# Optimization experiments

Hardware: AMD Instinct MI355X
Metric: run time of the kernel (lower is better)

## Reference

```python
import jax, jax.numpy as jnp
import numpy as np

N_NODES = 100000
IN_CH = 512
OUT_CH = 64
N_EDGES = 1600000
NEG_SLOPE = 0.2  # PyG GATv2Conv default negative_slope


def setup_inputs() -> dict:
    key = jax.random.key(0)
    ks = jax.random.split(key, 8)
    x = jax.random.normal(ks[0], (N_NODES, IN_CH), dtype=jnp.float32)
    edge_index = jax.random.randint(ks[1], (2, N_EDGES), 0, N_NODES, dtype=jnp.int64)
    s_in = 1.0 / np.sqrt(IN_CH)
    s_out = 1.0 / np.sqrt(OUT_CH)
    W_l = jax.random.uniform(ks[2], (IN_CH, OUT_CH), jnp.float32, -s_in, s_in)
    b_l = jnp.zeros((OUT_CH,), jnp.float32)
    W_r = jax.random.uniform(ks[3], (IN_CH, OUT_CH), jnp.float32, -s_in, s_in)
    b_r = jnp.zeros((OUT_CH,), jnp.float32)
    att = jax.random.uniform(ks[4], (OUT_CH,), jnp.float32, -s_out, s_out)
    bias = jnp.zeros((OUT_CH,), jnp.float32)
    return {"x": x, "edge_index": edge_index, "W_l": W_l, "b_l": b_l,
            "W_r": W_r, "b_r": b_r, "att": att, "bias": bias}


def reference(x, edge_index, W_l, b_l, W_r, b_r, att, bias):
    n = x.shape[0]
    # add self loops (PyG GATv2Conv default add_self_loops=True)
    loop = jnp.arange(n, dtype=edge_index.dtype)
    src = jnp.concatenate([edge_index[0], loop])  # source j
    dst = jnp.concatenate([edge_index[1], loop])  # target i

    x_l = x @ W_l + b_l  # [N, D] source-side transform
    x_r = x @ W_r + b_r  # [N, D] target-side transform

    # GATv2 attention logit per edge: att . LeakyReLU(x_l[j] + x_r[i])
    z = x_l[src] + x_r[dst]                       # [E, D]
    z = jnp.where(z > 0, z, NEG_SLOPE * z)
    logits = z @ att                               # [E]

    # segment softmax over incoming edges of each target node
    seg_max = jax.ops.segment_max(logits, dst, num_segments=n)
    seg_max = jnp.where(jnp.isfinite(seg_max), seg_max, 0.0)
    e = jnp.exp(logits - seg_max[dst])
    denom = jax.ops.segment_sum(e, dst, num_segments=n)
    alpha = e / jnp.maximum(denom[dst], 1e-16)     # [E]

    # weighted scatter-add aggregation of source features
    out = jax.ops.segment_sum(alpha[:, None] * x_l[src], dst, num_segments=n)
    return out + bias
```

## Files before the change

### kernel.cpp

```cpp
#include <hip/hip_runtime.h>
#include <hip/hip_bf16.h>

constexpr int IC = 512;
constexpr int OC = 64;
#define NEG_SLOPE 0.2f

constexpr int EPB = 4096;
constexpr int NBK = 128;
constexpr int BKSHIFT = 10;
constexpr int BKSIZE = 1024;

typedef __attribute__((ext_vector_type(8))) __bf16 bf16x8;
typedef __attribute__((ext_vector_type(4))) float f32x4;
typedef unsigned short u16;

__device__ __forceinline__ float bf2f(u16 h) {
  return __uint_as_float(((unsigned)h) << 16);
}

__global__ __launch_bounds__(256)
void k_shuffleB(const float* __restrict__ Wl, const float* __restrict__ Wr,
                __hip_bfloat16* __restrict__ Bp) {
  const int tid = blockIdx.x * 256 + threadIdx.x;
  if (tid >= 8 * 16 * 64) return;
  const int lane = tid & 63;
  const int kb = (tid >> 6) & 15;
  const int cb = tid >> 10;
  const int col = cb * 16 + (lane & 15);
  const int k0 = kb * 32 + (lane >> 4) * 8;
  const float* W = (col < OC) ? (Wl + col) : (Wr + (col - OC));
  bf16x8 v;
  #pragma unroll
  for (int j = 0; j < 8; ++j) v[j] = (__bf16)W[(size_t)(k0 + j) * OC];
  *(bf16x8*)(Bp + (size_t)tid * 8) = v;
}

__device__ inline bf16x8 cvt8(const float4& a, const float4& b) {
  bf16x8 r;
  r[0] = (__bf16)a.x; r[1] = (__bf16)a.y; r[2] = (__bf16)a.z; r[3] = (__bf16)a.w;
  r[4] = (__bf16)b.x; r[5] = (__bf16)b.y; r[6] = (__bf16)b.z; r[7] = (__bf16)b.w;
  return r;
}

__device__ __forceinline__ void gload_lds16(const float* g, const float* l) {
  __builtin_amdgcn_global_load_lds(
      (const __attribute__((address_space(1))) float*)(uintptr_t)g,
      (__attribute__((address_space(3))) float*)(uintptr_t)l,
      16, 0, 0);
}

__global__ __launch_bounds__(256)
void k_gemm(const float* __restrict__ x, const __hip_bfloat16* __restrict__ Bp,
            const float* __restrict__ bl, const float* __restrict__ br,
            __bf16* __restrict__ xl, __bf16* __restrict__ xr, int n) {
  __shared__ float As[2][128 * 64];
  const int t = threadIdx.x;
  const int lane = t & 63;
  const int w = t >> 6;
  const int l15 = lane & 15, lg = lane >> 4;
  const int rowbase_g = blockIdx.x * 128 + w * 32;

  const float* srcp[8];
  #pragma unroll
  for (int j = 0; j < 8; ++j) {
    const int row_l = w * 32 + j * 4 + lg;
    const int grow = min(blockIdx.x * 128 + row_l, n - 1);
    const int gch = l15 ^ ((j * 4 + lg) & 15);
    srcp[j] = x + (size_t)grow * IC + gch * 4;
  }
  const bf16x8* pb = (const bf16x8*)Bp + lane;

  f32x4 acc[2][8] = {};

  #pragma unroll
  for (int j = 0; j < 8; ++j)
    gload_lds16(srcp[j], &As[0][w * 2048 + j * 256]);

  int buf = 0;
  for (int kt = 0; kt < 8; ++kt) {
    bf16x8 bfr[2][8];
    #pragma unroll
    for (int kb = 0; kb < 2; ++kb)
      #pragma unroll
      for (int cb = 0; cb < 8; ++cb)
        bfr[kb][cb] = pb[(cb * 16 + kt * 2 + kb) * 64];
    asm volatile("s_waitcnt vmcnt(16)" ::: "memory");
    if (kt < 7) {
      #pragma unroll
      for (int j = 0; j < 8; ++j)
        gload_lds16(srcp[j] + (kt + 1) * 64, &As[buf ^ 1][w * 2048 + j * 256]);
    }
    #pragma unroll
    for (int kb = 0; kb < 2; ++kb) {
      const int kc0 = kb * 8 + lg * 2;
      const int s0 = (kc0 ^ l15) * 4;
      const int s1 = ((kc0 + 1) ^ l15) * 4;
      #pragma unroll
      for (int rg = 0; rg < 2; ++rg) {
        const int rbase = (w * 32 + rg * 16 + l15) * 64;
        const float4 f0 = *(const float4*)&As[buf][rbase + s0];
        const float4 f1 = *(const float4*)&As[buf][rbase + s1];
        const bf16x8 af = cvt8(f0, f1);
        #pragma unroll
        for (int cb = 0; cb < 8; ++cb)
          acc[rg][cb] = __builtin_amdgcn_mfma_f32_16x16x32_bf16(af, bfr[kb][cb], acc[rg][cb], 0, 0, 0);
      }
    }
    buf ^= 1;
  }

  #pragma unroll
  for (int cb = 0; cb < 8; ++cb) {
    const int col = cb * 16 + l15;
    __bf16* dst = (col < OC) ? xl : xr;
    const int c2 = col & (OC - 1);
    const float bv = (col < OC) ? bl[c2] : br[c2];
    #pragma unroll
    for (int rg = 0; rg < 2; ++rg) {
      const int rb = rowbase_g + rg * 16 + lg * 4;
      #pragma unroll
      for (int q = 0; q < 4; ++q)
        if (rb + q < n) dst[(size_t)(rb + q) * OC + c2] = (__bf16)(acc[rg][cb][q] + bv);
    }
  }
}

__global__ __launch_bounds__(256)
void k_bin1a(const int* __restrict__ edst, int* __restrict__ slen,
             int E, int nch) {
  __shared__ int lcnt[NBK];
  const int t = threadIdx.x;
  const int c = blockIdx.x;
  const int e0 = c * EPB;
  if (t < NBK) lcnt[t] = 0;
  __syncthreads();
  #pragma unroll
  for (int j = 0; j < 16; ++j) {
    const int i = e0 + j * 256 + t;
    if (i < E) atomicAdd(&lcnt[edst[i] >> BKSHIFT], 1);
  }
  __syncthreads();
  if (t < NBK) slen[t * nch + c] = lcnt[t];
}

__global__ __launch_bounds__(256)
void k_colscan(int* __restrict__ slen, int* __restrict__ btot, int nch) {
  __shared__ int sm[256];
  const int t = threadIdx.x;
  const int base = blockIdx.x * nch;
  const int per = (nch + 255) / 256;
  int v[8];
  int s = 0;
  for (int k = 0; k < per; ++k) {
    const int idx = t * per + k;
    v[k] = (idx < nch) ? slen[base + idx] : 0;
    s += v[k];
  }
  sm[t] = s;
  __syncthreads();
  #pragma unroll
  for (int d = 1; d < 256; d <<= 1) {
    int u = (t >= d) ? sm[t - d] : 0;
    __syncthreads();
    sm[t] += u;
    __syncthreads();
  }
  int run = (t == 0) ? 0 : sm[t - 1];
  for (int k = 0; k < per; ++k) {
    const int idx = t * per + k;
    if (idx < nch) slen[base + idx] = run;
    run += v[k];
  }
  if (t == 255) btot[blockIdx.x] = sm[255];
}

__global__ __launch_bounds__(256)
void k_bscan(const int* __restrict__ btot, int* __restrict__ bbase, int nbk) {
  __shared__ int sm[256];
  const int t = threadIdx.x;
  const int v = (t < nbk) ? btot[t] : 0;
  sm[t] = v;
  __syncthreads();
  #pragma unroll
  for (int d = 1; d < 256; d <<= 1) {
    int u = (t >= d) ? sm[t - d] : 0;
    __syncthreads();
    sm[t] += u;
    __syncthreads();
  }
  if (t < NBK) bbase[t] = sm[t] - v;
  if (t == NBK - 1) bbase[NBK] = sm[t];
}

__global__ __launch_bounds__(256)
void k_bin1b(const int* __restrict__ esrc, const int* __restrict__ edst,
             const int* __restrict__ slen, const int* __restrict__ bbase,
             int* __restrict__ bstage, int E, int nch) {
  __shared__ int lcnt[NBK];
  __shared__ int lbase[NBK];
  __shared__ int ldst[NBK];
  __shared__ int lword[EPB];
  __shared__ unsigned char lbkt[EPB];
  __shared__ int sm[256];
  const int t = threadIdx.x;
  const int c = blockIdx.x;
  const int e0 = c * EPB;
  if (t < NBK) lcnt[t] = 0;
  __syncthreads();

  int s_[16], d_[16], r_[16];
  #pragma unroll
  for (int j = 0; j < 16; ++j) {
    const int i = e0 + j * 256 + t;
    if (i < E) {
      s_[j] = esrc[i];
      d_[j] = edst[i];
      r_[j] = atomicAdd(&lcnt[d_[j] >> BKSHIFT], 1);
    }
  }
  __syncthreads();
  const int vv = (t < NBK) ? lcnt[t] : 0;
  sm[t] = vv;
  __syncthreads();
  #pragma unroll
  for (int d = 1; d < 256; d <<= 1) {
    int u = (t >= d) ? sm[t - d] : 0;
    __syncthreads();
    sm[t] += u;
    __syncthreads();
  }
  if (t < NBK) {
    lbase[t] = sm[t] - vv;
    ldst[t] = bbase[t] + slen[t * nch + c];
  }
  __syncthreads();
  #pragma unroll
  for (int j = 0; j < 16; ++j) {
    const int i = e0 + j * 256 + t;
    if (i < E) {
      const int b = d_[j] >> BKSHIFT;
      const int pos = lbase[b] + r_[j];
      lword[pos] = (s_[j] << BKSHIFT) | (d_[j] & (BKSIZE - 1));
      lbkt[pos] = (unsigned char)b;
    }
  }
  __syncthreads();
  const int used = min(E - e0, EPB);
  for (int k = t; k < used; k += 256) {
    const int b = lbkt[k];
    bstage[ldst[b] + (k - lbase[b])] = lword[k];
  }
}

__global__ __launch_bounds__(1024)
void k_boff(const int* __restrict__ bstage, const int* __restrict__ bbase,
            int* __restrict__ off, int n, int nbk) {
  __shared__ int lc[BKSIZE];
  __shared__ int sw[16];
  const int t = threadIdx.x;
  const int b = blockIdx.x;
  const int node0 = b << BKSHIFT;
  lc[t] = 0;
  __syncthreads();
  const int end = bbase[b + 1];
  for (int k = bbase[b] + t; k < end; k += 1024)
    atomicAdd(&lc[bstage[k] & (BKSIZE - 1)], 1);
  __syncthreads();
  const int v = lc[t];
  int sc = v;
  #pragma unroll
  for (int d = 1; d < 64; d <<= 1) {
    const int u = __shfl_up(sc, d);
    if ((t & 63) >= d) sc += u;
  }
  if ((t & 63) == 63) sw[t >> 6] = sc;
  __syncthreads();
  if (t < 64) {
    int s2 = (t < 16) ? sw[t] : 0;
    #pragma unroll
    for (int d = 1; d < 16; d <<= 1) {
      const int u = __shfl_up(s2, d);
      if (t >= d) s2 += u;
    }
    if (t < 16) sw[t] = s2;
  }
  __syncthreads();
  const int wbase = (t >= 64) ? sw[(t >> 6) - 1] : 0;
  const int node = node0 + t;
  if (node < n) off[node] = bbase[b] + node0 + t + (wbase + sc - v);
  if (b == nbk - 1 && t == 1023) off[n] = bbase[nbk] + n;
}

__global__ __launch_bounds__(1024)
void k_bplace(const int* __restrict__ bstage, const int* __restrict__ bbase,
              const int* __restrict__ off, int* __restrict__ rec, int n) {
  __shared__ int lcur[BKSIZE];
  const int t = threadIdx.x;
  const int b = blockIdx.x;
  const int node0 = b << BKSHIFT;
  if (node0 + t < n) {
    const int o = off[node0 + t];
    rec[o] = node0 + t;
    lcur[t] = o + 1;
  }
  __syncthreads();
  const int end = bbase[b + 1];
  for (int k = bbase[b] + t; k < end; k += 1024) {
    const int w = bstage[k];
    const int pos = atomicAdd(&lcur[w & (BKSIZE - 1)], 1);
    rec[pos] = w >> BKSHIFT;
  }
}

__global__ __launch_bounds__(256)
void k_gather(const int* __restrict__ off, const int* __restrict__ rec,
              const u16* __restrict__ xl, const u16* __restrict__ xr,
              const float* __restrict__ att, const float* __restrict__ bias,
              float* __restrict__ out, int n) {
  const int lane = threadIdx.x & 63;
  const int node = (blockIdx.x * 256 + threadIdx.x) >> 6;
  if (node >= n) return;
  const int slot = lane >> 4;
  const int c4 = (lane & 15) * 4;

  const ushort4 xrh = *(const ushort4*)(xr + (size_t)node * OC + c4);
  const float4 xrv = make_float4(bf2f(xrh.x), bf2f(xrh.y), bf2f(xrh.z), bf2f(xrh.w));
  const float4 aw  = *(const float4*)(att + c4);

  const int beg = off[node];
  const int end = off[node + 1];
  float denom = 0.0f;
  float4 acc = make_float4(0.f, 0.f, 0.f, 0.f);

  int p = beg + slot;
  bool cv = (p < end);
  ushort4 xh = make_ushort4(0, 0, 0, 0);
  if (cv) {
    const int s = rec[p];
    xh = *(const ushort4*)(xl + (size_t)s * OC + c4);
  }
  for (int base = beg; base < end; base += 4) {
    const ushort4 ch = xh;
    const bool curv = cv;
    p += 4;
    cv = (p < end);
    if (cv) {
      const int s = rec[p];
      xh = *(const ushort4*)(xl + (size_t)s * OC + c4);
    } else {
      xh = make_ushort4(0, 0, 0, 0);
    }
    const float4 cur = make_float4(bf2f(ch.x), bf2f(ch.y), bf2f(ch.z), bf2f(ch.w));
    float zx = cur.x + xrv.x; zx = zx > 0.f ? zx : NEG_SLOPE * zx;
    float zy = cur.y + xrv.y; zy = zy > 0.f ? zy : NEG_SLOPE * zy;
    float zz = cur.z + xrv.z; zz = zz > 0.f ? zz : NEG_SLOPE * zz;
    float zw = cur.w + xrv.w; zw = zw > 0.f ? zw : NEG_SLOPE * zw;
    float lg = zx * aw.x + zy * aw.y + zz * aw.z + zw * aw.w;
    lg += __shfl_xor(lg, 1);
    lg += __shfl_xor(lg, 2);
    lg += __shfl_xor(lg, 4);
    lg += __shfl_xor(lg, 8);
    const float wgt = curv ? __expf(lg) : 0.0f;
    denom += wgt;
    acc.x = fmaf(wgt, cur.x, acc.x);
    acc.y = fmaf(wgt, cur.y, acc.y);
    acc.z = fmaf(wgt, cur.z, acc.z);
    acc.w = fmaf(wgt, cur.w, acc.w);
  }
  denom += __shfl_xor(denom, 16);
  denom += __shfl_xor(denom, 32);
  acc.x += __shfl_xor(acc.x, 16); acc.x += __shfl_xor(acc.x, 32);
  acc.y += __shfl_xor(acc.y, 16); acc.y += __shfl_xor(acc.y, 32);
  acc.z += __shfl_xor(acc.z, 16); acc.z += __shfl_xor(acc.z, 32);
  acc.w += __shfl_xor(acc.w, 16); acc.w += __shfl_xor(acc.w, 32);

  if (slot == 0) {
    const float4 bv = *(const float4*)(bias + c4);
    const float inv = 1.0f / denom;
    float4 o;
    o.x = acc.x * inv + bv.x;
    o.y = acc.y * inv + bv.y;
    o.z = acc.z * inv + bv.z;
    o.w = acc.w * inv + bv.w;
    *(float4*)(out + (size_t)node * OC + c4) = o;
  }
}

extern "C" void kernel_launch(void* const* d_in, const int* in_sizes, int n_in,
                              void* d_out, int out_size, void* d_ws, size_t ws_size,
                              hipStream_t stream) {
  const float* x    = (const float*)d_in[0];
  const int*   ei   = (const int*)d_in[1];
  const float* Wl   = (const float*)d_in[2];
  const float* bl   = (const float*)d_in[3];
  const float* Wr   = (const float*)d_in[4];
  const float* br   = (const float*)d_in[5];
  const float* att  = (const float*)d_in[6];
  const float* bias = (const float*)d_in[7];
  float* out = (float*)d_out;

  const int n = in_sizes[0] / IC;
  const int E = in_sizes[1] / 2;
  const int total = E + n;
  const int* esrc = ei;
  const int* edst = ei + E;
  const int nch = (E + EPB - 1) / EPB;
  const int nbk = (n + BKSIZE - 1) >> BKSHIFT;

  char* wp = (char*)d_ws;
  __hip_bfloat16* Bp = (__hip_bfloat16*)wp;  wp += 131072;
  __bf16* xl  = (__bf16*)wp;                 wp += (size_t)n * OC * 2;
  __bf16* xr  = (__bf16*)wp;                 wp += (size_t)n * OC * 2;
  int* bstage = (int*)wp;                    wp += (size_t)E * 4;
  int* slen   = (int*)wp;                    wp += (size_t)NBK * nch * 4;
  int* btot   = (int*)wp;                    wp += (size_t)NBK * 4;
  int* bbase  = (int*)wp;                    wp += (size_t)(NBK + 1) * 4;
  int* off    = (int*)wp;                    wp += (size_t)(n + 1) * 4;
  int* rec    = (int*)wp;                    wp += (size_t)total * 4;

  k_shuffleB<<<32, 256, 0, stream>>>(Wl, Wr, Bp);
  k_gemm<<<(n + 127) / 128, 256, 0, stream>>>(x, Bp, bl, br, xl, xr, n);
  k_bin1a<<<nch, 256, 0, stream>>>(edst, slen, E, nch);
  k_colscan<<<nbk, 256, 0, stream>>>(slen, btot, nch);
  k_bscan<<<1, 256, 0, stream>>>(btot, bbase, nbk);
  k_bin1b<<<nch, 256, 0, stream>>>(esrc, edst, slen, bbase, bstage, E, nch);
  k_boff<<<nbk, 1024, 0, stream>>>(bstage, bbase, off, n, nbk);
  k_bplace<<<nbk, 1024, 0, stream>>>(bstage, bbase, off, rec, n);
  k_gather<<<((size_t)n * 64 + 255) / 256, 256, 0, stream>>>(off, rec, (const u16*)xl, (const u16*)xr, att, bias, out, n);
}
```

Before: 178.2 us.

## Fuse offset and placement kernels; widen gather to 8 edges per wavefront

Merges the per-bucket offset scan and the edge placement into one kernel, so the bucket's edge stream is read in the same launch and the offsets need not be reloaded. The gather kernel now processes 8 edges at a time with 8 lanes per edge holding 8 channels each. Each wavefront loads up to 64 neighbor indices with one coalesced read and distributes them with shuffles. This cuts launch overhead and dependent index loads and raises memory-level parallelism in the gather, at the cost of more registers per lane and wasted lanes for low-degree nodes.

```diff
diff --git a/kernel.cpp b/kernel.cpp
--- a/kernel.cpp
+++ b/kernel.cpp
@@ -12,6 +12,7 @@
 
 typedef __attribute__((ext_vector_type(8))) __bf16 bf16x8;
 typedef __attribute__((ext_vector_type(4))) float f32x4;
+typedef __attribute__((ext_vector_type(8))) unsigned short u16x8;
 typedef unsigned short u16;
 
 __device__ __forceinline__ float bf2f(u16 h) {
@@ -253,8 +254,8 @@
 }
 
 __global__ __launch_bounds__(1024)
-void k_boff(const int* __restrict__ bstage, const int* __restrict__ bbase,
-            int* __restrict__ off, int n, int nbk) {
+void k_boffplace(const int* __restrict__ bstage, const int* __restrict__ bbase,
+                 int* __restrict__ off, int* __restrict__ rec, int n, int nbk) {
   __shared__ int lc[BKSIZE];
   __shared__ int sw[16];
   const int t = threadIdx.x;
@@ -262,8 +263,9 @@
   const int node0 = b << BKSHIFT;
   lc[t] = 0;
   __syncthreads();
+  const int beg = bbase[b];
   const int end = bbase[b + 1];
-  for (int k = bbase[b] + t; k < end; k += 1024)
+  for (int k = beg + t; k < end; k += 1024)
     atomicAdd(&lc[bstage[k] & (BKSIZE - 1)], 1);
   __syncthreads();
   const int v = lc[t];
@@ -287,27 +289,18 @@
   __syncthreads();
   const int wbase = (t >= 64) ? sw[(t >> 6) - 1] : 0;
   const int node = node0 + t;
-  if (node < n) off[node] = bbase[b] + node0 + t + (wbase + sc - v);
+  int o = 0;
+  if (node < n) {
+    o = beg + node0 + t + (wbase + sc - v);
+    off[node] = o;
+    rec[o] = node;
+  }
   if (b == nbk - 1 && t == 1023) off[n] = bbase[nbk] + n;
-}
-
-__global__ __launch_bounds__(1024)
-void k_bplace(const int* __restrict__ bstage, const int* __restrict__ bbase,
-              const int* __restrict__ off, int* __restrict__ rec, int n) {
-  __shared__ int lcur[BKSIZE];
-  const int t = threadIdx.x;
-  const int b = blockIdx.x;
-  const int node0 = b << BKSHIFT;
-  if (node0 + t < n) {
-    const int o = off[node0 + t];
-    rec[o] = node0 + t;
-    lcur[t] = o + 1;
-  }
-  __syncthreads();
-  const int end = bbase[b + 1];
-  for (int k = bbase[b] + t; k < end; k += 1024) {
+  lc[t] = o + 1;
+  __syncthreads();
+  for (int k = beg + t; k < end; k += 1024) {
     const int w = bstage[k];
-    const int pos = atomicAdd(&lcur[w & (BKSIZE - 1)], 1);
+    const int pos = atomicAdd(&lc[w & (BKSIZE - 1)], 1);
     rec[pos] = w >> BKSHIFT;
   }
 }
@@ -320,69 +313,79 @@
   const int lane = threadIdx.x & 63;
   const int node = (blockIdx.x * 256 + threadIdx.x) >> 6;
   if (node >= n) return;
-  const int slot = lane >> 4;
-  const int c4 = (lane & 15) * 4;
-
-  const ushort4 xrh = *(const ushort4*)(xr + (size_t)node * OC + c4);
-  const float4 xrv = make_float4(bf2f(xrh.x), bf2f(xrh.y), bf2f(xrh.z), bf2f(xrh.w));
-  const float4 aw  = *(const float4*)(att + c4);
+  const int slot = lane >> 3;
+  const int c8 = (lane & 7) * 8;
+
+  const u16x8 xrh = *(const u16x8*)(xr + (size_t)node * OC + c8);
+  float xrv[8], aw[8];
+  #pragma unroll
+  for (int j = 0; j < 8; ++j) {
+    xrv[j] = bf2f(xrh[j]);
+    aw[j] = att[c8 + j];
+  }
 
   const int beg = off[node];
   const int end = off[node + 1];
   float denom = 0.0f;
-  float4 acc = make_float4(0.f, 0.f, 0.f, 0.f);
-
-  int p = beg + slot;
-  bool cv = (p < end);
-  ushort4 xh = make_ushort4(0, 0, 0, 0);
-  if (cv) {
-    const int s = rec[p];
-    xh = *(const ushort4*)(xl + (size_t)s * OC + c4);
-  }
-  for (int base = beg; base < end; base += 4) {
-    const ushort4 ch = xh;
-    const bool curv = cv;
-    p += 4;
-    cv = (p < end);
-    if (cv) {
-      const int s = rec[p];
-      xh = *(const ushort4*)(xl + (size_t)s * OC + c4);
-    } else {
-      xh = make_ushort4(0, 0, 0, 0);
-    }
-    const float4 cur = make_float4(bf2f(ch.x), bf2f(ch.y), bf2f(ch.z), bf2f(ch.w));
-    float zx = cur.x + xrv.x; zx = zx > 0.f ? zx : NEG_SLOPE * zx;
-    float zy = cur.y + xrv.y; zy = zy > 0.f ? zy : NEG_SLOPE * zy;
-    float zz = cur.z + xrv.z; zz = zz > 0.f ? zz : NEG_SLOPE * zz;
-    float zw = cur.w + xrv.w; zw = zw > 0.f ? zw : NEG_SLOPE * zw;
-    float lg = zx * aw.x + zy * aw.y + zz * aw.z + zw * aw.w;
-    lg += __shfl_xor(lg, 1);
-    lg += __shfl_xor(lg, 2);
-    lg += __shfl_xor(lg, 4);
-    lg += __shfl_xor(lg, 8);
-    const float wgt = curv ? __expf(lg) : 0.0f;
-    denom += wgt;
-    acc.x = fmaf(wgt, cur.x, acc.x);
-    acc.y = fmaf(wgt, cur.y, acc.y);
-    acc.z = fmaf(wgt, cur.z, acc.z);
-    acc.w = fmaf(wgt, cur.w, acc.w);
-  }
+  float acc[8] = {};
+
+  for (int c0 = beg; c0 < end; c0 += 64) {
+    const int cend = min(end - c0, 64);
+    int myrec = 0;
+    if (lane < cend) myrec = rec[c0 + lane];
+    int eidx = slot;
+    bool v = (eidx < cend);
+    int s = __shfl(myrec, eidx);
+    u16x8 xh = {};
+    if (v) xh = *(const u16x8*)(xl + (size_t)s * OC + c8);
+    for (int m = 0; m * 8 < cend; ++m) {
+      const u16x8 ch = xh;
+      const bool curv = v;
+      eidx += 8;
+      v = (eidx < cend);
+      s = __shfl(myrec, min(eidx, 63));
+      if (v) xh = *(const u16x8*)(xl + (size_t)s * OC + c8);
+      float cur[8];
+      float lg = 0.0f;
+      #pragma unroll
+      for (int j = 0; j < 8; ++j) {
+        cur[j] = bf2f(ch[j]);
+        float z = cur[j] + xrv[j];
+        z = z > 0.0f ? z : NEG_SLOPE * z;
+        lg = fmaf(z, aw[j], lg);
+      }
+      lg += __shfl_xor(lg, 1);
+      lg += __shfl_xor(lg, 2);
+      lg += __shfl_xor(lg, 4);
+      const float wgt = curv ? __expf(lg) : 0.0f;
+      denom += wgt;
+      #pragma unroll
+      for (int j = 0; j < 8; ++j) acc[j] = fmaf(wgt, cur[j], acc[j]);
+    }
+  }
+  denom += __shfl_xor(denom, 8);
   denom += __shfl_xor(denom, 16);
   denom += __shfl_xor(denom, 32);
-  acc.x += __shfl_xor(acc.x, 16); acc.x += __shfl_xor(acc.x, 32);
-  acc.y += __shfl_xor(acc.y, 16); acc.y += __shfl_xor(acc.y, 32);
-  acc.z += __shfl_xor(acc.z, 16); acc.z += __shfl_xor(acc.z, 32);
-  acc.w += __shfl_xor(acc.w, 16); acc.w += __shfl_xor(acc.w, 32);
+  #pragma unroll
+  for (int j = 0; j < 8; ++j) {
+    acc[j] += __shfl_xor(acc[j], 8);
+    acc[j] += __shfl_xor(acc[j], 16);
+    acc[j] += __shfl_xor(acc[j], 32);
+  }
 
   if (slot == 0) {
-    const float4 bv = *(const float4*)(bias + c4);
     const float inv = 1.0f / denom;
-    float4 o;
-    o.x = acc.x * inv + bv.x;
-    o.y = acc.y * inv + bv.y;
-    o.z = acc.z * inv + bv.z;
-    o.w = acc.w * inv + bv.w;
-    *(float4*)(out + (size_t)node * OC + c4) = o;
+    float4 o0, o1;
+    o0.x = acc[0] * inv + bias[c8 + 0];
+    o0.y = acc[1] * inv + bias[c8 + 1];
+    o0.z = acc[2] * inv + bias[c8 + 2];
+    o0.w = acc[3] * inv + bias[c8 + 3];
+    o1.x = acc[4] * inv + bias[c8 + 4];
+    o1.y = acc[5] * inv + bias[c8 + 5];
+    o1.z = acc[6] * inv + bias[c8 + 6];
+    o1.w = acc[7] * inv + bias[c8 + 7];
+    *(float4*)(out + (size_t)node * OC + c8) = o0;
+    *(float4*)(out + (size_t)node * OC + c8 + 4) = o1;
   }
 }
 
@@ -424,7 +427,6 @@
   k_colscan<<<nbk, 256, 0, stream>>>(slen, btot, nch);
   k_bscan<<<1, 256, 0, stream>>>(btot, bbase, nbk);
   k_bin1b<<<nch, 256, 0, stream>>>(esrc, edst, slen, bbase, bstage, E, nch);
-  k_boff<<<nbk, 1024, 0, stream>>>(bstage, bbase, off, n, nbk);
-  k_bplace<<<nbk, 1024, 0, stream>>>(bstage, bbase, off, rec, n);
+  k_boffplace<<<nbk, 1024, 0, stream>>>(bstage, bbase, off, rec, n, nbk);
   k_gather<<<((size_t)n * 64 + 255) / 256, 256, 0, stream>>>(off, rec, (const u16*)xl, (const u16*)xr, att, bias, out, n);
 }
```

Result: faster. 169.3 us (-5.0%).
